# Performance work log

Measured on AMD Instinct MI355X. Metric: run time of the kernel, lower is better.

Reference implementation:

```python
import jax, jax.numpy as jnp
import numpy as np

LEAK = 0.2
TEMP = 0.1          # CausalMask temperature
SPARSITY_W = 0.1
MI_W = 0.01
DAG_W = 1.0

def _leaky(x):
    return jax.nn.leaky_relu(x, LEAK)

def setup_inputs() -> dict:
    key = jax.random.key(0)
    B, F, S, H = 4096, 512, 32, 512
    H2, CH = H // 2, 64
    P = S * (S - 1) // 2  # 496 MI estimators
    ks = jax.random.split(key, 32)
    def w(k, shape, fan_in):
        return jax.random.normal(k, shape, jnp.float32) / np.sqrt(fan_in)
    return {
        'features': jax.random.normal(ks[0], (B, F), jnp.float32),
        'eps':      jax.random.normal(ks[1], (B, S), jnp.float32),
        'enc_w1': w(ks[2], (F, H), F),   'enc_b1': w(ks[3], (H,), H),
        'enc_w2': w(ks[4], (H, 2 * S), H), 'enc_b2': w(ks[5], (2 * S,), H) * 0.1,
        'log_weight': jax.random.normal(ks[6], (S, S), jnp.float32) * 0.5,
        'mech_w1': w(ks[7], (S, S, H2), S), 'mech_b1': w(ks[8], (S, H2), H2),
        'mech_w2': w(ks[9], (S, H2), H2),   'mech_b2': w(ks[10], (S,), H2),
        'dec_w1': w(ks[11], (S, H), S),  'dec_b1': w(ks[12], (H,), H),
        'dec_w2': w(ks[13], (H, F), H),  'dec_b2': w(ks[14], (F,), H),
        'mi_w1': w(ks[15], (P, 2, CH), 2),  'mi_b1': w(ks[16], (P, CH), CH),
        'mi_w2': w(ks[17], (P, CH, CH), CH), 'mi_b2': w(ks[18], (P, CH), CH),
        'mi_w3': w(ks[19], (P, CH), CH),     'mi_b3': w(ks[20], (P,), CH),
    }

def _forward(features, eps, enc_w1, enc_b1, enc_w2, enc_b2, log_weight,
             mech_w1, mech_b1, mech_w2, mech_b2, dec_w1, dec_b1, dec_w2, dec_b2,
             mi_w1, mi_b1, mi_w2, mi_b2, mi_w3, mi_b3):
    S = log_weight.shape[0]
    # ---- encode ----
    h = _leaky(features @ enc_w1 + enc_b1)
    params = h @ enc_w2 + enc_b2
    mean, log_std = jnp.split(params, 2, axis=-1)
    std = jnp.exp(log_std)
    z = mean + std * eps                                   # [B,S]
    # ---- soft causal adjacency (training mode) ----
    eye = jnp.eye(S, dtype=features.dtype)
    upper = jnp.triu(jnp.ones((S, S), features.dtype), k=1)
    lw = log_weight * upper - 10.0 * eye
    A = jax.nn.sigmoid(lw / TEMP)                          # [S,S]
    # ---- apply_causal_structure: stoch_dim tiny MLPs, vectorized ----
    # z_parents[b,i,s] = z[b,s] * A[s,i]
    zp = z[:, None, :] * A.T[None, :, :]                   # [B,S,S]
    h1 = _leaky(jnp.einsum('bis,ish->bih', zp, mech_w1) + mech_b1)  # [B,S,H2]
    z_causal = jnp.einsum('bih,ih->bi', h1, mech_w2) + mech_b2      # [B,S]
    # ---- decode ----
    recon = _leaky(z_causal @ dec_w1 + dec_b1) @ dec_w2 + dec_b2    # [B,F]
    # ---- losses ----
    recon_loss = jnp.mean((recon - features) ** 2)
    kl_loss = 0.5 * jnp.sum(mean ** 2 + std ** 2 - 2.0 * log_std - 1.0, axis=-1).mean()
    Asig = jax.nn.sigmoid(log_weight)
    sparsity_loss = jnp.sum(jnp.abs(Asig))
    # MI: one tiny MLP per (i<j) pair, row-major order == torch loop order
    iu, ju = jnp.triu_indices(S, k=1)
    pair = jnp.stack([z[:, iu], z[:, ju]], axis=-1)        # [B,P,2]
    m1 = _leaky(jnp.einsum('bpi,pih->bph', pair, mi_w1) + mi_b1)
    m2 = _leaky(jnp.einsum('bph,phk->bpk', m1, mi_w2) + mi_b2)
    mi_est = (jnp.einsum('bph,ph->bp', m2, mi_w3) + mi_b3).mean(0)  # [P]
    mi_loss = jnp.sum(jax.nn.sigmoid(log_weight[iu, ju]) * mi_est)
    # DAG: truncated matrix-exponential trace penalty
    A2 = Asig * Asig
    expm = eye
    mp = eye
    fact = 1.0
    for i in range(1, 10):
        fact *= i
        mp = mp @ A2
        expm = expm + mp / fact
    dag_loss = (jnp.trace(expm) - S) ** 2
    total_loss = recon_loss + kl_loss + SPARSITY_W * sparsity_loss + MI_W * mi_loss + DAG_W * dag_loss
    return z_causal, mean, std, recon, total_loss, recon_loss, kl_loss, sparsity_loss, mi_loss, dag_loss

def reference(features, eps, enc_w1, enc_b1, enc_w2, enc_b2, log_weight,
              mech_w1, mech_b1, mech_w2, mech_b2, dec_w1, dec_b1, dec_w2, dec_b2,
              mi_w1, mi_b1, mi_w2, mi_b2, mi_w3, mi_b3):
    return _forward(features, eps, enc_w1, enc_b1, enc_w2, enc_b2, log_weight,
                    mech_w1, mech_b1, mech_w2, mech_b2, dec_w1, dec_b1, dec_w2, dec_b2,
                    mi_w1, mi_b1, mi_w2, mi_b2, mi_w3, mi_b3)
```

## Files before the change

kernel.cpp:

```cpp
#include <hip/hip_runtime.h>
#include <hip/hip_bf16.h>

typedef float f32x4 __attribute__((ext_vector_type(4)));
typedef short s16x8 __attribute__((ext_vector_type(8)));

__device__ __forceinline__ float leaky2(float x){ return fmaf(0.4f, fabsf(x), 0.6f * x); }

__device__ __forceinline__ short f2bf(float f){
    return __builtin_bit_cast(short, __float2bfloat16(f));
}

__global__ void k_setup(const float* __restrict__ lw, float* __restrict__ A,
                        float* __restrict__ acc)
{
    __shared__ float A2s[1024], mp[1024], red[1024];
    const int t = threadIdx.x;
    const int r = t >> 5, c = t & 31;
    float v = lw[t];
    float sig = 1.f / (1.f + expf(-v));
    float l2 = (r < c) ? v * 10.f : ((r == c) ? -100.f : 0.f);
    A[t] = 1.f / (1.f + expf(-l2));
    red[t] = sig;
    float a2 = sig * sig;
    A2s[t] = a2; mp[t] = a2;
    __syncthreads();
    for (int s = 512; s > 0; s >>= 1){ if (t < s) red[t] += red[t + s]; __syncthreads(); }
    if (t == 0) acc[2] = red[0];

    const float invf[10] = {0.f, 1.f, 0.5f, 1.6666667e-1f, 4.1666667e-2f,
                            8.3333333e-3f, 1.3888889e-3f, 1.9841270e-4f,
                            2.4801587e-5f, 2.7557319e-6f};
    float tr = 0.f;
    for (int n = 1; n <= 9; ++n){
        __syncthreads();
        if (t == 0){
            float s = 0.f;
            for (int k2 = 0; k2 < 32; ++k2) s += mp[k2 * 33];
            tr += s * invf[n];
        }
        if (n == 9) break;
        float a = 0.f;
        for (int k2 = 0; k2 < 32; ++k2) a += mp[r * 32 + k2] * A2s[k2 * 32 + c];
        __syncthreads();
        mp[t] = a;
    }
    if (t == 0) acc[3] = tr * tr;
}

__global__ void k_cvt(const float* __restrict__ feat, const float* __restrict__ ew1,
                      const float* __restrict__ ew2, const float* __restrict__ dw2,
                      const float* __restrict__ mw1,
                      short* __restrict__ featbf, short* __restrict__ w1p,
                      short* __restrict__ ew2p, short* __restrict__ dw2p,
                      short* __restrict__ mw1p)
{
    for (int idx = blockIdx.x * 256 + threadIdx.x; idx < 2916352; idx += gridDim.x * 256){
        if (idx < 2097152){ featbf[idx] = f2bf(feat[idx]); continue; }
        int j = idx - 2097152;
        if (j < 262144){
            int q = j & 511, t = j >> 9, lane = q >> 3, e = q & 7, kt = t & 15, nt = t >> 4;
            int k = kt * 32 + (lane >> 4) * 8 + e, n = nt * 16 + (lane & 15);
            w1p[j] = f2bf(ew1[k * 512 + n]); continue;
        }
        j -= 262144;
        if (j < 32768){
            int q = j & 511, t = j >> 9, lane = q >> 3, e = q & 7, kt = t & 15, nt = t >> 4;
            int k = kt * 32 + (lane >> 4) * 8 + e, n = nt * 16 + (lane & 15);
            ew2p[j] = f2bf(ew2[k * 64 + n]); continue;
        }
        j -= 32768;
        if (j < 262144){
            int q = j & 511, t = j >> 9, lane = q >> 3, e = q & 7, kt = t & 15, nt = t >> 4;
            int k = kt * 32 + (lane >> 4) * 8 + e, n = nt * 16 + (lane & 15);
            dw2p[j] = f2bf(dw2[k * 512 + n]); continue;
        }
        j -= 262144;
        int i = j >> 13, q2 = j & 8191, nt = q2 >> 9, w = q2 & 511, lane = w >> 3, e = w & 7;
        int k = (lane >> 4) * 8 + e, col = nt * 16 + (lane & 15);
        mw1p[j] = f2bf(mw1[(i * 32 + k) * 256 + col]);
    }
}

__global__ __launch_bounds__(256) void k_genc(const short* __restrict__ Abf,
                                              const short* __restrict__ Bp,
                                              const float* __restrict__ bias,
                                              short* __restrict__ Hbf)
{
    const int lane = threadIdx.x & 63, wv = threadIdx.x >> 6;
    const int ml = lane & 15, kg = lane >> 4;
    const int b0 = blockIdx.x * 64 + (wv >> 1) * 32;
    const int c0 = blockIdx.y * 128 + (wv & 1) * 64;
    const int nt0 = c0 >> 4;
    f32x4 acc[2][4] = {};
    for (int kt = 0; kt < 16; ++kt){
        s16x8 a[2], b[4];
        #pragma unroll
        for (int mi = 0; mi < 2; ++mi)
            a[mi] = *(const s16x8*)&Abf[(size_t)(b0 + mi * 16 + ml) * 512 + kt * 32 + kg * 8];
        #pragma unroll
        for (int ni = 0; ni < 4; ++ni)
            b[ni] = *(const s16x8*)&Bp[((nt0 + ni) * 16 + kt) * 512 + lane * 8];
        #pragma unroll
        for (int mi = 0; mi < 2; ++mi)
            #pragma unroll
            for (int ni = 0; ni < 4; ++ni)
                acc[mi][ni] = __builtin_amdgcn_mfma_f32_16x16x32_bf16(a[mi], b[ni], acc[mi][ni], 0, 0, 0);
    }
    #pragma unroll
    for (int ni = 0; ni < 4; ++ni){
        int col = c0 + ni * 16 + ml;
        float bv = bias[col];
        #pragma unroll
        for (int mi = 0; mi < 2; ++mi)
            #pragma unroll
            for (int r = 0; r < 4; ++r){
                int row = b0 + mi * 16 + kg * 4 + r;
                Hbf[(size_t)row * 512 + col] = f2bf(leaky2(acc[mi][ni][r] + bv));
            }
    }
}

__global__ __launch_bounds__(256) void k_grec(const short* __restrict__ Abf,
                                              const short* __restrict__ Bp,
                                              const float* __restrict__ bias,
                                              const float* __restrict__ feat,
                                              float* __restrict__ recon,
                                              float* __restrict__ accg)
{
    __shared__ float red[256];
    const int t = threadIdx.x;
    const int lane = t & 63, wv = t >> 6;
    const int ml = lane & 15, kg = lane >> 4;
    const int b0 = blockIdx.x * 64 + (wv >> 1) * 32;
    const int c0 = blockIdx.y * 128 + (wv & 1) * 64;
    const int nt0 = c0 >> 4;
    f32x4 acc[2][4] = {};
    for (int kt = 0; kt < 16; ++kt){
        s16x8 a[2], b[4];
        #pragma unroll
        for (int mi = 0; mi < 2; ++mi)
            a[mi] = *(const s16x8*)&Abf[(size_t)(b0 + mi * 16 + ml) * 512 + kt * 32 + kg * 8];
        #pragma unroll
        for (int ni = 0; ni < 4; ++ni)
            b[ni] = *(const s16x8*)&Bp[((nt0 + ni) * 16 + kt) * 512 + lane * 8];
        #pragma unroll
        for (int mi = 0; mi < 2; ++mi)
            #pragma unroll
            for (int ni = 0; ni < 4; ++ni)
                acc[mi][ni] = __builtin_amdgcn_mfma_f32_16x16x32_bf16(a[mi], b[ni], acc[mi][ni], 0, 0, 0);
    }
    float lsum = 0.f;
    #pragma unroll
    for (int ni = 0; ni < 4; ++ni){
        int col = c0 + ni * 16 + ml;
        float bv = bias[col];
        #pragma unroll
        for (int mi = 0; mi < 2; ++mi)
            #pragma unroll
            for (int r = 0; r < 4; ++r){
                int row = b0 + mi * 16 + kg * 4 + r;
                float v = acc[mi][ni][r] + bv;
                float d = v - feat[(size_t)row * 512 + col];
                lsum = fmaf(d, d, lsum);
                recon[(size_t)row * 512 + col] = v;
            }
    }
    red[t] = lsum; __syncthreads();
    for (int s = 128; s > 0; s >>= 1){ if (t < s) red[t] += red[t + s]; __syncthreads(); }
    if (t == 0) atomicAdd(accg + 1, red[0]);
}

__global__ __launch_bounds__(256) void k_pmfma(const short* __restrict__ Hbf,
                                               const short* __restrict__ Bp,
                                               const float* __restrict__ b2,
                                               const float* __restrict__ eps,
                                               float* __restrict__ omean,
                                               float* __restrict__ ostd,
                                               float* __restrict__ zbuf,
                                               float* __restrict__ accg)
{
    __shared__ float P[16][65];
    __shared__ float red[256];
    const int t = threadIdx.x, lane = t & 63, wv = t >> 6;
    const int ml = lane & 15, kg = lane >> 4;
    const int b0 = blockIdx.x * 16;
    f32x4 acc = {};
    for (int kt = 0; kt < 16; ++kt){
        s16x8 b = *(const s16x8*)&Bp[(wv * 16 + kt) * 512 + lane * 8];
        s16x8 a = *(const s16x8*)&Hbf[(size_t)(b0 + ml) * 512 + kt * 32 + kg * 8];
        acc = __builtin_amdgcn_mfma_f32_16x16x32_bf16(a, b, acc, 0, 0, 0);
    }
    {
        int col = wv * 16 + ml;
        float bv = b2[col];
        #pragma unroll
        for (int r = 0; r < 4; ++r)
            P[kg * 4 + r][col] = acc[r] + bv;
    }
    __syncthreads();
    float klp = 0.f;
    #pragma unroll
    for (int q = 0; q < 2; ++q){
        int e = q * 256 + t;
        int row = e >> 5, n = e & 31;
        float mean = P[row][n], ls = P[row][n + 32];
        float sd = expf(ls);
        size_t o = (size_t)(b0 + row) * 32 + n;
        float z = fmaf(sd, eps[o], mean);
        omean[o] = mean; ostd[o] = sd; zbuf[o] = z;
        klp += mean * mean + sd * sd - 2.f * ls - 1.f;
    }
    red[t] = klp; __syncthreads();
    for (int s = 128; s > 0; s >>= 1){ if (t < s) red[t] += red[t + s]; __syncthreads(); }
    if (t == 0) atomicAdd(accg + 0, red[0]);
}

__global__ __launch_bounds__(256) void k_mechm(const float* __restrict__ z,
                                               const float* __restrict__ A,
                                               const short* __restrict__ W1p,
                                               const float* __restrict__ b1,
                                               const float* __restrict__ w2,
                                               const float* __restrict__ b2,
                                               float* __restrict__ out_zc,
                                               float* __restrict__ zcbuf)
{
    __shared__ float sA[32], sB1[256], sW2[256];
    const int t = threadIdx.x, lane = t & 63, wv = t >> 6;
    const int ml = lane & 15, kg = lane >> 4;
    const int i = blockIdx.y;
    const int b0 = blockIdx.x * 64 + wv * 16;
    if (t < 32) sA[t] = A[t * 32 + i];
    sB1[t] = b1[i * 256 + t];
    sW2[t] = w2[i * 256 + t];
    __syncthreads();
    const f32x4* zr = (const f32x4*)&z[(size_t)(b0 + ml) * 32 + kg * 8];
    f32x4 z0 = zr[0], z1 = zr[1];
    s16x8 af;
    #pragma unroll
    for (int q = 0; q < 4; ++q){
        af[q]     = f2bf(z0[q] * sA[kg * 8 + q]);
        af[q + 4] = f2bf(z1[q] * sA[kg * 8 + 4 + q]);
    }
    float s[4] = {0.f, 0.f, 0.f, 0.f};
    #pragma unroll
    for (int nt = 0; nt < 16; ++nt){
        s16x8 bf = *(const s16x8*)&W1p[i * 8192 + nt * 512 + lane * 8];
        int col = nt * 16 + ml;
        float b1v = sB1[col], w2v = sW2[col];
        f32x4 d = {b1v, b1v, b1v, b1v};
        d = __builtin_amdgcn_mfma_f32_16x16x32_bf16(af, bf, d, 0, 0, 0);
        float w2a = 0.6f * w2v, w2b = 0.4f * w2v;
        #pragma unroll
        for (int r = 0; r < 4; ++r)
            s[r] = fmaf(w2a, d[r], fmaf(w2b, fabsf(d[r]), s[r]));
    }
    #pragma unroll
    for (int off = 1; off < 16; off <<= 1)
        #pragma unroll
        for (int r = 0; r < 4; ++r) s[r] += __shfl_xor(s[r], off);
    if (ml == 0){
        float bb = b2[i];
        #pragma unroll
        for (int r = 0; r < 4; ++r){
            int b = b0 + kg * 4 + r;
            float zc = s[r] + bb;
            out_zc[(size_t)b * 32 + i] = zc;
            zcbuf [(size_t)b * 32 + i] = zc;
        }
    }
}

__global__ __launch_bounds__(256) void k_dec1(
    const float* __restrict__ zc, const float* __restrict__ w1,
    const float* __restrict__ b1, short* __restrict__ d1)
{
    int gid = blockIdx.x * 256 + threadIdx.x;
    int b = gid >> 9, hc = gid & 511;
    const f32x4* z4 = (const f32x4*)(zc + (size_t)b * 32);
    float a = b1[hc];
    #pragma unroll
    for (int q = 0; q < 8; ++q){
        f32x4 v = z4[q];
        a = fmaf(v[0], w1[(q * 4 + 0) * 512 + hc], a);
        a = fmaf(v[1], w1[(q * 4 + 1) * 512 + hc], a);
        a = fmaf(v[2], w1[(q * 4 + 2) * 512 + hc], a);
        a = fmaf(v[3], w1[(q * 4 + 3) * 512 + hc], a);
    }
    d1[(size_t)b * 512 + hc] = f2bf(leaky2(a));
}

__global__ __launch_bounds__(256) void k_mi(
    const float* __restrict__ z, const float* __restrict__ w1g,
    const float* __restrict__ b1g, const float* __restrict__ w2g,
    const float* __restrict__ b2g, const float* __restrict__ w3g,
    float* __restrict__ macc)
{
    const int p = blockIdx.x >> 2, bq = blockIdx.x & 3;
    const int lane = threadIdx.x & 63, wv = threadIdx.x >> 6;
    const int ml = lane & 15, kg = lane >> 4;
    int pi = 0, rem = p;
    while (rem >= 31 - pi){ rem -= 31 - pi; ++pi; }
    const int pj = pi + 1 + rem;

    float w10s[2][8], w11s[2][8], b1s[2][8];
    s16x8 bfr[4][2];
    float w3a[4], w3b[4], b2r[4];
    #pragma unroll
    for (int ks = 0; ks < 2; ++ks)
        #pragma unroll
        for (int i2 = 0; i2 < 8; ++i2){
            int h = ks * 32 + kg * 8 + i2;
            w10s[ks][i2] = 0.6f * w1g[p * 128 + h];
            w11s[ks][i2] = 0.6f * w1g[p * 128 + 64 + h];
            b1s[ks][i2]  = 0.6f * b1g[p * 64 + h];
        }
    #pragma unroll
    for (int nb = 0; nb < 4; ++nb){
        float w3 = w3g[p * 64 + nb * 16 + ml];
        w3a[nb] = 0.6f * w3; w3b[nb] = 0.4f * w3;
        b2r[nb] = b2g[p * 64 + nb * 16 + ml];
        #pragma unroll
        for (int ks = 0; ks < 2; ++ks)
            #pragma unroll
            for (int i2 = 0; i2 < 8; ++i2){
                int h = ks * 32 + kg * 8 + i2;
                bfr[nb][ks][i2] = f2bf(w2g[(size_t)p * 4096 + h * 64 + nb * 16 + ml]);
            }
    }
    float s = 0.f;
    for (int tile = 0; tile < 16; ++tile){
        int b = bq * 1024 + (tile * 4 + wv) * 16 + ml;
        float zi = z[(size_t)b * 32 + pi], zj = z[(size_t)b * 32 + pj];
        s16x8 af[2];
        #pragma unroll
        for (int ks = 0; ks < 2; ++ks)
            #pragma unroll
            for (int i2 = 0; i2 < 8; ++i2){
                float m = fmaf(zi, w10s[ks][i2], fmaf(zj, w11s[ks][i2], b1s[ks][i2]));
                m = fmaf(0.66666669f, fabsf(m), m);
                af[ks][i2] = f2bf(m);
            }
        #pragma unroll
        for (int nb = 0; nb < 4; ++nb){
            f32x4 d = {b2r[nb], b2r[nb], b2r[nb], b2r[nb]};
            d = __builtin_amdgcn_mfma_f32_16x16x32_bf16(af[0], bfr[nb][0], d, 0, 0, 0);
            d = __builtin_amdgcn_mfma_f32_16x16x32_bf16(af[1], bfr[nb][1], d, 0, 0, 0);
            #pragma unroll
            for (int r2 = 0; r2 < 4; ++r2)
                s = fmaf(w3a[nb], d[r2], fmaf(w3b[nb], fabsf(d[r2]), s));
        }
    }
    #pragma unroll
    for (int off = 32; off; off >>= 1) s += __shfl_xor(s, off);
    if (lane == 0) atomicAdd(&macc[p], s);
}

__global__ void k_final(const float* __restrict__ acc, const float* __restrict__ lw,
                        const float* __restrict__ b3, float* __restrict__ outs)
{
    __shared__ float red[512];
    int t = threadIdx.x;
    float c = 0.f;
    if (t < 496){
        int pi = 0, rem = t;
        while (rem >= 31 - pi){ rem -= 31 - pi; ++pi; }
        int pj = pi + 1 + rem;
        float est = acc[4 + t] * (1.f / 4096.f) + b3[t];
        float w = 1.f / (1.f + expf(-lw[pi * 32 + pj]));
        c = w * est;
    }
    red[t] = c; __syncthreads();
    for (int s = 256; s > 0; s >>= 1){ if (t < s) red[t] += red[t + s]; __syncthreads(); }
    if (t == 0){
        float mi    = red[0];
        float recon = acc[1] * (1.f / (4096.f * 512.f));
        float kl    = 0.5f * acc[0] * (1.f / 4096.f);
        float sp    = acc[2], dag = acc[3];
        outs[0] = recon + kl + 0.1f * sp + 0.01f * mi + dag;
        outs[1] = recon; outs[2] = kl; outs[3] = sp; outs[4] = mi; outs[5] = dag;
    }
}

extern "C" void kernel_launch(void* const* d_in, const int* in_sizes, int n_in,
                              void* d_out, int out_size, void* d_ws, size_t ws_size,
                              hipStream_t stream)
{
    const float* features = (const float*)d_in[0];
    const float* eps      = (const float*)d_in[1];
    const float* enc_w1   = (const float*)d_in[2];
    const float* enc_b1   = (const float*)d_in[3];
    const float* enc_w2   = (const float*)d_in[4];
    const float* enc_b2   = (const float*)d_in[5];
    const float* log_w    = (const float*)d_in[6];
    const float* mech_w1  = (const float*)d_in[7];
    const float* mech_b1  = (const float*)d_in[8];
    const float* mech_w2  = (const float*)d_in[9];
    const float* mech_b2  = (const float*)d_in[10];
    const float* dec_w1   = (const float*)d_in[11];
    const float* dec_b1   = (const float*)d_in[12];
    const float* dec_w2   = (const float*)d_in[13];
    const float* dec_b2   = (const float*)d_in[14];
    const float* mi_w1    = (const float*)d_in[15];
    const float* mi_b1    = (const float*)d_in[16];
    const float* mi_w2    = (const float*)d_in[17];
    const float* mi_b2    = (const float*)d_in[18];
    const float* mi_w3    = (const float*)d_in[19];
    const float* mi_b3    = (const float*)d_in[20];

    float* W      = (float*)d_ws;
    float* zbuf   = W;
    float* zcbuf  = W + 131072;
    float* Abuf   = W + 262144;
    float* accums = W + 263168;
    short* w1p    = (short*)(W + 263680);
    short* ew2p   = (short*)(W + 394752);
    short* dw2p   = (short*)(W + 411136);
    short* mw1p   = (short*)(W + 542208);
    short* d1bf   = (short*)(W + 673280);
    float* out    = (float*)d_out;
    short* featbf = (short*)(out + 393216);
    short* hbf    = (short*)(out + 393216 + 1048576);

    hipMemsetAsync(accums, 0, 512 * sizeof(float), stream);
    k_setup<<<1, 1024, 0, stream>>>(log_w, Abuf, accums);
    k_cvt<<<2048, 256, 0, stream>>>(features, enc_w1, enc_w2, dec_w2, mech_w1,
                                    featbf, w1p, ew2p, dw2p, mw1p);
    k_genc<<<dim3(64, 4), 256, 0, stream>>>(featbf, w1p, enc_b1, hbf);
    k_pmfma<<<256, 256, 0, stream>>>(hbf, ew2p, enc_b2, eps,
                                     out + 131072, out + 262144, zbuf, accums);
    k_mechm<<<dim3(64, 32), 256, 0, stream>>>(zbuf, Abuf, mw1p, mech_b1,
                                              mech_w2, mech_b2, out, zcbuf);
    k_dec1<<<8192, 256, 0, stream>>>(zcbuf, dec_w1, dec_b1, d1bf);
    k_grec<<<dim3(64, 4), 256, 0, stream>>>(d1bf, dw2p, dec_b2, features,
                                            out + 393216, accums);
    k_mi<<<1984, 256, 0, stream>>>(zbuf, mi_w1, mi_b1, mi_w2, mi_b2, mi_w3, accums + 4);
    k_final<<<1, 512, 0, stream>>>(accums, log_w, mi_b3, out + 2490368);
}
```

Before: 139.0 us.

## Fuse MI estimator and mechanism kernels, transpose z, prepack MI weights to bf16

Merges the MI-estimator and causal-mechanism kernels into one launch whose blocks branch on blockIdx, so the two independent workloads share the GPU at the same time. z is now written transposed (stoch-dim major) so that per-pair loads read contiguous batch rows. mi_w2 is converted to bf16 in MFMA fragment layout inside the conversion kernel, which removes per-block strided gathers. The MI inner loop also keeps separate linear and absolute sums and applies w3 only at the end. The packed mi_w2 reuses the d1bf buffer, which is safe only because the decoder writes d1bf after the fused kernel has finished.

```diff
diff --git a/kernel.cpp b/kernel.cpp
--- a/kernel.cpp
+++ b/kernel.cpp
@@ -49,12 +49,12 @@
 
 __global__ void k_cvt(const float* __restrict__ feat, const float* __restrict__ ew1,
                       const float* __restrict__ ew2, const float* __restrict__ dw2,
-                      const float* __restrict__ mw1,
+                      const float* __restrict__ mw1, const float* __restrict__ mw2,
                       short* __restrict__ featbf, short* __restrict__ w1p,
                       short* __restrict__ ew2p, short* __restrict__ dw2p,
-                      short* __restrict__ mw1p)
-{
-    for (int idx = blockIdx.x * 256 + threadIdx.x; idx < 2916352; idx += gridDim.x * 256){
+                      short* __restrict__ mw1p, short* __restrict__ mw2p)
+{
+    for (int idx = blockIdx.x * 256 + threadIdx.x; idx < 4947968; idx += gridDim.x * 256){
         if (idx < 2097152){ featbf[idx] = f2bf(feat[idx]); continue; }
         int j = idx - 2097152;
         if (j < 262144){
@@ -75,9 +75,16 @@
             dw2p[j] = f2bf(dw2[k * 512 + n]); continue;
         }
         j -= 262144;
-        int i = j >> 13, q2 = j & 8191, nt = q2 >> 9, w = q2 & 511, lane = w >> 3, e = w & 7;
-        int k = (lane >> 4) * 8 + e, col = nt * 16 + (lane & 15);
-        mw1p[j] = f2bf(mw1[(i * 32 + k) * 256 + col]);
+        if (j < 262144){
+            int i = j >> 13, q2 = j & 8191, nt = q2 >> 9, w = q2 & 511, lane = w >> 3, e = w & 7;
+            int k = (lane >> 4) * 8 + e, col = nt * 16 + (lane & 15);
+            mw1p[j] = f2bf(mw1[(i * 32 + k) * 256 + col]); continue;
+        }
+        j -= 262144;
+        int p2 = j >> 12, q2 = j & 4095, tt = q2 >> 9, w = q2 & 511, lane = w >> 3, e = w & 7;
+        int nb = tt >> 1, ks = tt & 1;
+        int k2 = ks * 32 + (lane >> 4) * 8 + e, col = nb * 16 + (lane & 15);
+        mw2p[j] = f2bf(mw2[(size_t)p2 * 4096 + k2 * 64 + col]);
     }
 }
 
@@ -176,10 +183,11 @@
                                                const float* __restrict__ eps,
                                                float* __restrict__ omean,
                                                float* __restrict__ ostd,
-                                               float* __restrict__ zbuf,
+                                               float* __restrict__ zt,
                                                float* __restrict__ accg)
 {
     __shared__ float P[16][65];
+    __shared__ float zs[16][33];
     __shared__ float red[256];
     const int t = threadIdx.x, lane = t & 63, wv = t >> 6;
     const int ml = lane & 15, kg = lane >> 4;
@@ -207,65 +215,149 @@
         float sd = expf(ls);
         size_t o = (size_t)(b0 + row) * 32 + n;
         float z = fmaf(sd, eps[o], mean);
-        omean[o] = mean; ostd[o] = sd; zbuf[o] = z;
+        omean[o] = mean; ostd[o] = sd;
+        zs[row][n] = z;
         klp += mean * mean + sd * sd - 2.f * ls - 1.f;
+    }
+    __syncthreads();
+    #pragma unroll
+    for (int q = 0; q < 2; ++q){
+        int e = q * 256 + t;
+        int n = e >> 4, row = e & 15;
+        zt[(size_t)n * 4096 + b0 + row] = zs[row][n];
     }
     red[t] = klp; __syncthreads();
     for (int s = 128; s > 0; s >>= 1){ if (t < s) red[t] += red[t + s]; __syncthreads(); }
     if (t == 0) atomicAdd(accg + 0, red[0]);
 }
 
-__global__ __launch_bounds__(256) void k_mechm(const float* __restrict__ z,
-                                               const float* __restrict__ A,
-                                               const short* __restrict__ W1p,
-                                               const float* __restrict__ b1,
-                                               const float* __restrict__ w2,
-                                               const float* __restrict__ b2,
-                                               float* __restrict__ out_zc,
-                                               float* __restrict__ zcbuf)
-{
-    __shared__ float sA[32], sB1[256], sW2[256];
-    const int t = threadIdx.x, lane = t & 63, wv = t >> 6;
+__global__ __launch_bounds__(256) void k_mimech(
+    const float* __restrict__ zt,
+    const float* __restrict__ w1g, const float* __restrict__ b1g,
+    const short* __restrict__ w2p, const float* __restrict__ b2g,
+    const float* __restrict__ w3g, float* __restrict__ macc,
+    const float* __restrict__ A, const short* __restrict__ W1p,
+    const float* __restrict__ mb1, const float* __restrict__ mw2,
+    const float* __restrict__ mb2, float* __restrict__ out_zc,
+    float* __restrict__ zcbuf)
+{
+    const int lane = threadIdx.x & 63, wv = threadIdx.x >> 6;
     const int ml = lane & 15, kg = lane >> 4;
-    const int i = blockIdx.y;
-    const int b0 = blockIdx.x * 64 + wv * 16;
-    if (t < 32) sA[t] = A[t * 32 + i];
-    sB1[t] = b1[i * 256 + t];
-    sW2[t] = w2[i * 256 + t];
-    __syncthreads();
-    const f32x4* zr = (const f32x4*)&z[(size_t)(b0 + ml) * 32 + kg * 8];
-    f32x4 z0 = zr[0], z1 = zr[1];
-    s16x8 af;
-    #pragma unroll
-    for (int q = 0; q < 4; ++q){
-        af[q]     = f2bf(z0[q] * sA[kg * 8 + q]);
-        af[q + 4] = f2bf(z1[q] * sA[kg * 8 + 4 + q]);
-    }
-    float s[4] = {0.f, 0.f, 0.f, 0.f};
-    #pragma unroll
-    for (int nt = 0; nt < 16; ++nt){
-        s16x8 bf = *(const s16x8*)&W1p[i * 8192 + nt * 512 + lane * 8];
-        int col = nt * 16 + ml;
-        float b1v = sB1[col], w2v = sW2[col];
-        f32x4 d = {b1v, b1v, b1v, b1v};
-        d = __builtin_amdgcn_mfma_f32_16x16x32_bf16(af, bf, d, 0, 0, 0);
-        float w2a = 0.6f * w2v, w2b = 0.4f * w2v;
-        #pragma unroll
-        for (int r = 0; r < 4; ++r)
-            s[r] = fmaf(w2a, d[r], fmaf(w2b, fabsf(d[r]), s[r]));
-    }
-    #pragma unroll
-    for (int off = 1; off < 16; off <<= 1)
-        #pragma unroll
-        for (int r = 0; r < 4; ++r) s[r] += __shfl_xor(s[r], off);
-    if (ml == 0){
-        float bb = b2[i];
-        #pragma unroll
-        for (int r = 0; r < 4; ++r){
-            int b = b0 + kg * 4 + r;
-            float zc = s[r] + bb;
-            out_zc[(size_t)b * 32 + i] = zc;
-            zcbuf [(size_t)b * 32 + i] = zc;
+    if (blockIdx.x < 1984){
+        const int p = blockIdx.x >> 2, bq = blockIdx.x & 3;
+        int pi = 0, rem = p;
+        while (rem >= 31 - pi){ rem -= 31 - pi; ++pi; }
+        const int pj = pi + 1 + rem;
+
+        const float* zi_b = zt + (size_t)pi * 4096 + bq * 1024 + wv * 16 + ml;
+        const float* zj_b = zt + (size_t)pj * 4096 + bq * 1024 + wv * 16 + ml;
+        float ziv[16], zjv[16];
+        #pragma unroll
+        for (int t2 = 0; t2 < 16; ++t2){ ziv[t2] = zi_b[t2 * 64]; zjv[t2] = zj_b[t2 * 64]; }
+
+        float w10s[2][8], w11s[2][8], b1s[2][8];
+        #pragma unroll
+        for (int ks = 0; ks < 2; ++ks){
+            f32x4 a0 = *(const f32x4*)&w1g[p * 128 + ks * 32 + kg * 8];
+            f32x4 a1 = *(const f32x4*)&w1g[p * 128 + ks * 32 + kg * 8 + 4];
+            f32x4 c0 = *(const f32x4*)&w1g[p * 128 + 64 + ks * 32 + kg * 8];
+            f32x4 c1 = *(const f32x4*)&w1g[p * 128 + 64 + ks * 32 + kg * 8 + 4];
+            f32x4 d0 = *(const f32x4*)&b1g[p * 64 + ks * 32 + kg * 8];
+            f32x4 d1 = *(const f32x4*)&b1g[p * 64 + ks * 32 + kg * 8 + 4];
+            #pragma unroll
+            for (int q = 0; q < 4; ++q){
+                w10s[ks][q] = 0.6f * a0[q]; w10s[ks][q + 4] = 0.6f * a1[q];
+                w11s[ks][q] = 0.6f * c0[q]; w11s[ks][q + 4] = 0.6f * c1[q];
+                b1s[ks][q]  = 0.6f * d0[q]; b1s[ks][q + 4]  = 0.6f * d1[q];
+            }
+        }
+        s16x8 bfr[4][2];
+        float b2r[4];
+        #pragma unroll
+        for (int nb = 0; nb < 4; ++nb){
+            b2r[nb] = b2g[p * 64 + nb * 16 + ml];
+            #pragma unroll
+            for (int ks = 0; ks < 2; ++ks)
+                bfr[nb][ks] = *(const s16x8*)&w2p[(size_t)p * 4096 + (nb * 2 + ks) * 512 + lane * 8];
+        }
+        float slin[4] = {0.f, 0.f, 0.f, 0.f}, sabs[4] = {0.f, 0.f, 0.f, 0.f};
+        #pragma unroll
+        for (int tile = 0; tile < 16; ++tile){
+            s16x8 af0, af1;
+            #pragma unroll
+            for (int i2 = 0; i2 < 8; ++i2){
+                float m0 = fmaf(ziv[tile], w10s[0][i2], fmaf(zjv[tile], w11s[0][i2], b1s[0][i2]));
+                m0 = fmaf(0.66666669f, fabsf(m0), m0);
+                af0[i2] = f2bf(m0);
+                float m1 = fmaf(ziv[tile], w10s[1][i2], fmaf(zjv[tile], w11s[1][i2], b1s[1][i2]));
+                m1 = fmaf(0.66666669f, fabsf(m1), m1);
+                af1[i2] = f2bf(m1);
+            }
+            #pragma unroll
+            for (int nb = 0; nb < 4; ++nb){
+                f32x4 d = {b2r[nb], b2r[nb], b2r[nb], b2r[nb]};
+                d = __builtin_amdgcn_mfma_f32_16x16x32_bf16(af0, bfr[nb][0], d, 0, 0, 0);
+                d = __builtin_amdgcn_mfma_f32_16x16x32_bf16(af1, bfr[nb][1], d, 0, 0, 0);
+                #pragma unroll
+                for (int r2 = 0; r2 < 4; ++r2){
+                    slin[nb] += d[r2];
+                    sabs[nb] += fabsf(d[r2]);
+                }
+            }
+        }
+        float s = 0.f;
+        #pragma unroll
+        for (int nb = 0; nb < 4; ++nb){
+            float w3 = w3g[p * 64 + nb * 16 + ml];
+            s = fmaf(0.6f * w3, slin[nb], fmaf(0.4f * w3, sabs[nb], s));
+        }
+        #pragma unroll
+        for (int off = 32; off; off >>= 1) s += __shfl_xor(s, off);
+        if (lane == 0) atomicAdd(&macc[p], s);
+    } else {
+        __shared__ float sA[32], sB1[256], sW2[256];
+        const int bx = blockIdx.x - 1984;
+        const int i = bx & 31;
+        const int b0 = (bx >> 5) * 64 + wv * 16;
+        const int t = threadIdx.x;
+        if (t < 32) sA[t] = A[t * 32 + i];
+        sB1[t] = mb1[i * 256 + t];
+        sW2[t] = mw2[i * 256 + t];
+        __syncthreads();
+        float zv[8];
+        #pragma unroll
+        for (int q = 0; q < 8; ++q)
+            zv[q] = zt[(size_t)(kg * 8 + q) * 4096 + b0 + ml];
+        s16x8 af;
+        #pragma unroll
+        for (int q = 0; q < 8; ++q)
+            af[q] = f2bf(zv[q] * sA[kg * 8 + q]);
+        float s[4] = {0.f, 0.f, 0.f, 0.f};
+        #pragma unroll
+        for (int nt = 0; nt < 16; ++nt){
+            s16x8 bf = *(const s16x8*)&W1p[i * 8192 + nt * 512 + lane * 8];
+            int col = nt * 16 + ml;
+            float b1v = sB1[col], w2v = sW2[col];
+            f32x4 d = {b1v, b1v, b1v, b1v};
+            d = __builtin_amdgcn_mfma_f32_16x16x32_bf16(af, bf, d, 0, 0, 0);
+            float w2a = 0.6f * w2v, w2b = 0.4f * w2v;
+            #pragma unroll
+            for (int r = 0; r < 4; ++r)
+                s[r] = fmaf(w2a, d[r], fmaf(w2b, fabsf(d[r]), s[r]));
+        }
+        #pragma unroll
+        for (int off = 1; off < 16; off <<= 1)
+            #pragma unroll
+            for (int r = 0; r < 4; ++r) s[r] += __shfl_xor(s[r], off);
+        if (ml == 0){
+            float bb = mb2[i];
+            #pragma unroll
+            for (int r = 0; r < 4; ++r){
+                int b = b0 + kg * 4 + r;
+                float zc = s[r] + bb;
+                out_zc[(size_t)b * 32 + i] = zc;
+                zcbuf [(size_t)b * 32 + i] = zc;
+            }
         }
     }
 }
@@ -287,72 +379,6 @@
         a = fmaf(v[3], w1[(q * 4 + 3) * 512 + hc], a);
     }
     d1[(size_t)b * 512 + hc] = f2bf(leaky2(a));
-}
-
-__global__ __launch_bounds__(256) void k_mi(
-    const float* __restrict__ z, const float* __restrict__ w1g,
-    const float* __restrict__ b1g, const float* __restrict__ w2g,
-    const float* __restrict__ b2g, const float* __restrict__ w3g,
-    float* __restrict__ macc)
-{
-    const int p = blockIdx.x >> 2, bq = blockIdx.x & 3;
-    const int lane = threadIdx.x & 63, wv = threadIdx.x >> 6;
-    const int ml = lane & 15, kg = lane >> 4;
-    int pi = 0, rem = p;
-    while (rem >= 31 - pi){ rem -= 31 - pi; ++pi; }
-    const int pj = pi + 1 + rem;
-
-    float w10s[2][8], w11s[2][8], b1s[2][8];
-    s16x8 bfr[4][2];
-    float w3a[4], w3b[4], b2r[4];
-    #pragma unroll
-    for (int ks = 0; ks < 2; ++ks)
-        #pragma unroll
-        for (int i2 = 0; i2 < 8; ++i2){
-            int h = ks * 32 + kg * 8 + i2;
-            w10s[ks][i2] = 0.6f * w1g[p * 128 + h];
-            w11s[ks][i2] = 0.6f * w1g[p * 128 + 64 + h];
-            b1s[ks][i2]  = 0.6f * b1g[p * 64 + h];
-        }
-    #pragma unroll
-    for (int nb = 0; nb < 4; ++nb){
-        float w3 = w3g[p * 64 + nb * 16 + ml];
-        w3a[nb] = 0.6f * w3; w3b[nb] = 0.4f * w3;
-        b2r[nb] = b2g[p * 64 + nb * 16 + ml];
-        #pragma unroll
-        for (int ks = 0; ks < 2; ++ks)
-            #pragma unroll
-            for (int i2 = 0; i2 < 8; ++i2){
-                int h = ks * 32 + kg * 8 + i2;
-                bfr[nb][ks][i2] = f2bf(w2g[(size_t)p * 4096 + h * 64 + nb * 16 + ml]);
-            }
-    }
-    float s = 0.f;
-    for (int tile = 0; tile < 16; ++tile){
-        int b = bq * 1024 + (tile * 4 + wv) * 16 + ml;
-        float zi = z[(size_t)b * 32 + pi], zj = z[(size_t)b * 32 + pj];
-        s16x8 af[2];
-        #pragma unroll
-        for (int ks = 0; ks < 2; ++ks)
-            #pragma unroll
-            for (int i2 = 0; i2 < 8; ++i2){
-                float m = fmaf(zi, w10s[ks][i2], fmaf(zj, w11s[ks][i2], b1s[ks][i2]));
-                m = fmaf(0.66666669f, fabsf(m), m);
-                af[ks][i2] = f2bf(m);
-            }
-        #pragma unroll
-        for (int nb = 0; nb < 4; ++nb){
-            f32x4 d = {b2r[nb], b2r[nb], b2r[nb], b2r[nb]};
-            d = __builtin_amdgcn_mfma_f32_16x16x32_bf16(af[0], bfr[nb][0], d, 0, 0, 0);
-            d = __builtin_amdgcn_mfma_f32_16x16x32_bf16(af[1], bfr[nb][1], d, 0, 0, 0);
-            #pragma unroll
-            for (int r2 = 0; r2 < 4; ++r2)
-                s = fmaf(w3a[nb], d[r2], fmaf(w3b[nb], fabsf(d[r2]), s));
-        }
-    }
-    #pragma unroll
-    for (int off = 32; off; off >>= 1) s += __shfl_xor(s, off);
-    if (lane == 0) atomicAdd(&macc[p], s);
 }
 
 __global__ void k_final(const float* __restrict__ acc, const float* __restrict__ lw,
@@ -408,7 +434,7 @@
     const float* mi_b3    = (const float*)d_in[20];
 
     float* W      = (float*)d_ws;
-    float* zbuf   = W;
+    float* zt     = W;
     float* zcbuf  = W + 131072;
     float* Abuf   = W + 262144;
     float* accums = W + 263168;
@@ -417,22 +443,22 @@
     short* dw2p   = (short*)(W + 411136);
     short* mw1p   = (short*)(W + 542208);
     short* d1bf   = (short*)(W + 673280);
+    short* mw2p   = d1bf;
     float* out    = (float*)d_out;
     short* featbf = (short*)(out + 393216);
     short* hbf    = (short*)(out + 393216 + 1048576);
 
     hipMemsetAsync(accums, 0, 512 * sizeof(float), stream);
     k_setup<<<1, 1024, 0, stream>>>(log_w, Abuf, accums);
-    k_cvt<<<2048, 256, 0, stream>>>(features, enc_w1, enc_w2, dec_w2, mech_w1,
-                                    featbf, w1p, ew2p, dw2p, mw1p);
+    k_cvt<<<2048, 256, 0, stream>>>(features, enc_w1, enc_w2, dec_w2, mech_w1, mi_w2,
+                                    featbf, w1p, ew2p, dw2p, mw1p, mw2p);
     k_genc<<<dim3(64, 4), 256, 0, stream>>>(featbf, w1p, enc_b1, hbf);
     k_pmfma<<<256, 256, 0, stream>>>(hbf, ew2p, enc_b2, eps,
-                                     out + 131072, out + 262144, zbuf, accums);
-    k_mechm<<<dim3(64, 32), 256, 0, stream>>>(zbuf, Abuf, mw1p, mech_b1,
-                                              mech_w2, mech_b2, out, zcbuf);
+                                     out + 131072, out + 262144, zt, accums);
+    k_mimech<<<4032, 256, 0, stream>>>(zt, mi_w1, mi_b1, mw2p, mi_b2, mi_w3, accums + 4,
+                                       Abuf, mw1p, mech_b1, mech_w2, mech_b2, out, zcbuf);
     k_dec1<<<8192, 256, 0, stream>>>(zcbuf, dec_w1, dec_b1, d1bf);
     k_grec<<<dim3(64, 4), 256, 0, stream>>>(d1bf, dw2p, dec_b2, features,
                                             out + 393216, accums);
-    k_mi<<<1984, 256, 0, stream>>>(zbuf, mi_w1, mi_b1, mi_w2, mi_b2, mi_w3, accums + 4);
     k_final<<<1, 512, 0, stream>>>(accums, log_w, mi_b3, out + 2490368);
 }
```

Measured after the change: 151.6 us. 1.09x slower.
